# Kernel optimization log

Hardware: AMD Instinct MI355X
Metric: run time of the kernel (lower is better)

Reference implementation:

```python
import jax, jax.numpy as jnp
from jax import lax
import numpy as np

B, L, D_MODEL = 4, 2048, 1024
D_STATE, D_CONV, EXPAND = 16, 4, 2
D_INNER = EXPAND * D_MODEL          # 2048
DT_RANK = D_MODEL // 16             # 64
LN_EPS = 1e-5


def setup_inputs() -> dict:
    key = jax.random.key(0)
    ks = jax.random.split(key, 8)
    s = 0.02
    # S4D-real init for A_log, as in Mamba
    A_init = jnp.tile(jnp.arange(1, D_STATE + 1, dtype=jnp.float32), (D_INNER, 1))
    return {
        "x": jax.random.normal(ks[0], (B, L, D_MODEL), jnp.float32),
        "ln_g": jnp.ones((D_MODEL,), jnp.float32),
        "ln_b": jnp.zeros((D_MODEL,), jnp.float32),
        "W_in": jax.random.normal(ks[1], (D_MODEL, 2 * D_INNER), jnp.float32) * s,
        "conv_w": jax.random.normal(ks[2], (D_INNER, D_CONV), jnp.float32) * s,
        "conv_b": jnp.zeros((D_INNER,), jnp.float32),
        "W_x": jax.random.normal(ks[3], (D_INNER, DT_RANK + 2 * D_STATE), jnp.float32) * s,
        "W_dt": jax.random.normal(ks[4], (DT_RANK, D_INNER), jnp.float32) * s,
        "b_dt": jnp.full((D_INNER,), -4.6, jnp.float32),  # softplus(b_dt) ~ 0.01
        "A_log": jnp.log(A_init),
        "Dskip": jnp.ones((D_INNER,), jnp.float32),
        "W_out": jax.random.normal(ks[5], (D_INNER, D_MODEL), jnp.float32) * s,
    }


def _layer_norm(x, g, b):
    mu = jnp.mean(x, -1, keepdims=True)
    var = jnp.mean((x - mu) ** 2, -1, keepdims=True)
    return (x - mu) * lax.rsqrt(var + LN_EPS) * g + b


def _mamba_block(x, ln_g, ln_b, W_in, conv_w, conv_b, W_x, W_dt, b_dt, A_log, Dskip, W_out):
    b, l, _ = x.shape
    xn = _layer_norm(x, ln_g, ln_b)

    # in_proj -> (u, z), each (B, L, d_inner)
    xz = xn @ W_in
    u, z = jnp.split(xz, 2, axis=-1)

    # causal depthwise conv over L + SiLU
    u_t = u.transpose(0, 2, 1)                      # (B, d_inner, L)
    k = conv_w[:, None, :]                          # (d_inner, 1, d_conv)
    uc = lax.conv_general_dilated(
        u_t, k, (1,), [(D_CONV - 1, 0)],
        dimension_numbers=("NCH", "OIH", "NCH"),
        feature_group_count=D_INNER,
    ) + conv_b[None, :, None]
    uc = jax.nn.silu(uc).transpose(0, 2, 1)         # (B, L, d_inner)

    # input-dependent dt, B, C
    dbc = uc @ W_x                                  # (B, L, dt_rank + 2*d_state)
    dt_r = dbc[..., :DT_RANK]
    Bs = dbc[..., DT_RANK:DT_RANK + D_STATE]        # (B, L, d_state)
    Cs = dbc[..., DT_RANK + D_STATE:]               # (B, L, d_state)
    dt = jax.nn.softplus(dt_r @ W_dt + b_dt)        # (B, L, d_inner)

    A = -jnp.exp(A_log)                             # (d_inner, d_state)

    def step(h, ins):
        dt_t, B_t, C_t, u_t = ins                   # (b,di),(b,ds),(b,ds),(b,di)
        dA = jnp.exp(dt_t[..., None] * A)           # (b, di, ds)
        h = h * dA + (dt_t * u_t)[..., None] * B_t[:, None, :]
        y = jnp.einsum("bds,bs->bd", h, C_t)
        return h, y

    h0 = jnp.zeros((b, D_INNER, D_STATE), x.dtype)
    xs = (dt.transpose(1, 0, 2), Bs.transpose(1, 0, 2),
          Cs.transpose(1, 0, 2), uc.transpose(1, 0, 2))
    _, ys = lax.scan(step, h0, xs)                  # (L, B, d_inner)
    y = ys.transpose(1, 0, 2) + uc * Dskip          # D skip connection
    y = y * jax.nn.silu(z)                          # gate
    return x + y @ W_out                            # residual (dropout=0)


def reference(x, ln_g, ln_b, W_in, conv_w, conv_b, W_x, W_dt, b_dt, A_log, Dskip, W_out):
    return _mamba_block(x, ln_g, ln_b, W_in, conv_w, conv_b, W_x, W_dt, b_dt, A_log, Dskip, W_out)
```

## Files before the change

kernel.cpp:

```cpp
#include <hip/hip_runtime.h>
#include <hip/hip_bf16.h>

#define BB 4
#define LL 2048
#define DM 1024
#define DI 2048
#define DST 16
#define DTR 64
#define ROWS (BB*LL)
#define NC 32
#define CHUNK (LL/NC)

using bf16x8 = __attribute__((ext_vector_type(8))) __bf16;
using f32x4  = __attribute__((ext_vector_type(4))) float;

#define AS1 __attribute__((address_space(1)))
#define AS3 __attribute__((address_space(3)))

__global__ __launch_bounds__(256) void transpose_bf16_kernel(const float* __restrict__ src,
                                                             __hip_bfloat16* __restrict__ dst,
                                                             int R, int C, int Cpad) {
    __shared__ float t[32][33];
    const int c0 = blockIdx.x * 32, r0 = blockIdx.y * 32;
    const int tx = threadIdx.x & 31, ty = threadIdx.x >> 5;
    #pragma unroll
    for (int k = 0; k < 4; k++) {
        const int r = r0 + ty + 8 * k, c = c0 + tx;
        t[ty + 8 * k][tx] = (r < R && c < C) ? src[(size_t)r * C + c] : 0.f;
    }
    __syncthreads();
    #pragma unroll
    for (int k = 0; k < 4; k++) {
        const int c = c0 + ty + 8 * k, r = r0 + tx;
        if (c < Cpad && r < R) dst[(size_t)c * R + r] = __float2bfloat16(t[tx][ty + 8 * k]);
    }
}

__global__ __launch_bounds__(256) void ln_bf16_kernel(const float* __restrict__ x,
                                                      const float* __restrict__ g,
                                                      const float* __restrict__ bta,
                                                      __hip_bfloat16* __restrict__ xn) {
    const int row = blockIdx.x;
    const int tid = threadIdx.x;
    const float4 v = ((const float4*)(x + (size_t)row * DM))[tid];
    float s  = v.x + v.y + v.z + v.w;
    float sq = v.x*v.x + v.y*v.y + v.z*v.z + v.w*v.w;
    #pragma unroll
    for (int m = 1; m < 64; m <<= 1) {
        s  += __shfl_xor(s, m);
        sq += __shfl_xor(sq, m);
    }
    __shared__ float ss[4], ssq[4];
    const int w = tid >> 6;
    if ((tid & 63) == 0) { ss[w] = s; ssq[w] = sq; }
    __syncthreads();
    s  = ss[0] + ss[1] + ss[2] + ss[3];
    sq = ssq[0] + ssq[1] + ssq[2] + ssq[3];
    const float mu  = s * (1.f / DM);
    const float var = sq * (1.f / DM) - mu * mu;
    const float rs  = rsqrtf(var + 1e-5f);
    const float4 gv = ((const float4*)g)[tid];
    const float4 bv = ((const float4*)bta)[tid];
    __hip_bfloat16* op = xn + (size_t)row * DM + tid * 4;
    op[0] = __float2bfloat16((v.x - mu) * rs * gv.x + bv.x);
    op[1] = __float2bfloat16((v.y - mu) * rs * gv.y + bv.y);
    op[2] = __float2bfloat16((v.z - mu) * rs * gv.z + bv.z);
    op[3] = __float2bfloat16((v.w - mu) * rs * gv.w + bv.w);
}

template<int MODE>
__global__ __launch_bounds__(256) void mfma_gemm(const __hip_bfloat16* __restrict__ A,
                                                 const __hip_bfloat16* __restrict__ Bt,
                                                 float* __restrict__ O,
                                                 __hip_bfloat16* __restrict__ Oz,
                                                 __hip_bfloat16* __restrict__ Ozb,
                                                 const float* __restrict__ Add,
                                                 int K) {
    __shared__ __hip_bfloat16 As[2 * 128 * 32];
    __shared__ __hip_bfloat16 Bs[2 * 128 * 32];
    const int tid  = threadIdx.x;
    const int lane = tid & 63;
    const int w    = tid >> 6;

    const int nbx = gridDim.x, nby = gridDim.y;
    const int lid  = blockIdx.y * nbx + blockIdx.x;
    const int span = 8 * nbx;
    const int grp  = lid / span;
    const int fm0  = grp * 8;
    const int gsz  = min(nby - fm0, 8);
    const int by   = fm0 + (lid % gsz);
    const int bx   = (lid % span) / gsz;

    const int row0 = by * 128, col0 = bx * 128;
    const int wr0 = (w >> 1) * 64, wc0 = (w & 1) * 64;

    f32x4 acc[4][4];
    #pragma unroll
    for (int i = 0; i < 4; i++)
        #pragma unroll
        for (int j = 0; j < 4; j++) acc[i][j] = f32x4{0.f, 0.f, 0.f, 0.f};

    const int fm = lane & 15;
    const int fq = (lane >> 4) * 8;

    for (int k0 = 0; k0 < K; k0 += 64) {
        #pragma unroll
        for (int j = 0; j < 4; j++) {
            const int c   = w * 256 + j * 64 + lane;
            const int p   = c >> 9;
            const int row = (c >> 2) & 127;
            const int kq  = (c & 3) * 8;
            const int gk  = k0 + p * 32 + kq;
            __builtin_amdgcn_global_load_lds(
                (const AS1 unsigned int*)(A + (size_t)(row0 + row) * K + gk),
                (AS3 unsigned int*)(As + c * 8), 16, 0, 0);
            __builtin_amdgcn_global_load_lds(
                (const AS1 unsigned int*)(Bt + (size_t)(col0 + row) * K + gk),
                (AS3 unsigned int*)(Bs + c * 8), 16, 0, 0);
        }
        __syncthreads();
        #pragma unroll
        for (int half = 0; half < 2; half++) {
            bf16x8 af[4], bfr[4];
            #pragma unroll
            for (int i = 0; i < 4; i++)
                af[i] = *(const bf16x8*)&As[half * 4096 + (wr0 + i * 16 + fm) * 32 + fq];
            #pragma unroll
            for (int j = 0; j < 4; j++)
                bfr[j] = *(const bf16x8*)&Bs[half * 4096 + (wc0 + j * 16 + fm) * 32 + fq];
            #pragma unroll
            for (int i = 0; i < 4; i++)
                #pragma unroll
                for (int j = 0; j < 4; j++)
                    acc[i][j] = __builtin_amdgcn_mfma_f32_16x16x32_bf16(af[i], bfr[j], acc[i][j], 0, 0, 0);
        }
        __syncthreads();
    }

    #pragma unroll
    for (int i = 0; i < 4; i++) {
        #pragma unroll
        for (int j = 0; j < 4; j++) {
            #pragma unroll
            for (int r = 0; r < 4; r++) {
                const int row = row0 + wr0 + i * 16 + (lane >> 4) * 4 + r;
                const int col = col0 + wc0 + j * 16 + fm;
                const float v = acc[i][j][r];
                if (MODE == 0) {
                    if (col0 < DI) Oz[(size_t)row * DI + col] = __float2bfloat16(v);
                    else           Ozb[(size_t)row * DI + (col - DI)] = __float2bfloat16(v);
                } else if (MODE == 1) {
                    if (col >= DTR && col < DTR + 2 * DST)
                        O[(size_t)row * 128 + col] = v;
                    else if (col < DTR)
                        Oz[(size_t)row * DTR + col] = __float2bfloat16(v);
                } else if (MODE == 2) {
                    O[(size_t)row * DM + col] = v + Add[(size_t)row * DM + col];
                } else {
                    const float t  = v + Add[col];
                    const float sp = (t > 20.f) ? t : __logf(1.f + __expf(t));
                    Oz[(size_t)row * DI + col] = __float2bfloat16(sp);
                }
            }
        }
    }
}

__global__ __launch_bounds__(256) void conv_silu_kernel(const __hip_bfloat16* __restrict__ u,
                                                        const float* __restrict__ cw,
                                                        const float* __restrict__ cb,
                                                        __hip_bfloat16* __restrict__ uc) {
    const int d  = blockIdx.x * 256 + threadIdx.x;
    const int b  = blockIdx.z;
    const int l0 = blockIdx.y * 16;
    const float w0 = cw[d * 4 + 0], w1 = cw[d * 4 + 1];
    const float w2 = cw[d * 4 + 2], w3 = cw[d * 4 + 3];
    const float bias = cb[d];
    const __hip_bfloat16* up = u + (size_t)(b * LL) * DI + d;
    float x0 = (l0 - 3 >= 0) ? __bfloat162float(up[(size_t)(l0 - 3) * DI]) : 0.f;
    float x1 = (l0 - 2 >= 0) ? __bfloat162float(up[(size_t)(l0 - 2) * DI]) : 0.f;
    float x2 = (l0 - 1 >= 0) ? __bfloat162float(up[(size_t)(l0 - 1) * DI]) : 0.f;
    __hip_bfloat16* op = uc + (size_t)(b * LL + l0) * DI + d;
    #pragma unroll
    for (int i = 0; i < 16; i++) {
        const float x3 = __bfloat162float(up[(size_t)(l0 + i) * DI]);
        const float v  = bias + w0 * x0 + w1 * x1 + w2 * x2 + w3 * x3;
        const float sig = __builtin_amdgcn_rcpf(1.f + __expf(-v));
        op[(size_t)i * DI] = __float2bfloat16(v * sig);
        x0 = x1; x1 = x2; x2 = x3;
    }
}

__global__ __launch_bounds__(256) void scan_pass1_kernel(const __hip_bfloat16* __restrict__ dtb,
                                                         const __hip_bfloat16* __restrict__ uc,
                                                         const float* __restrict__ dbc,
                                                         const float* __restrict__ A_log,
                                                         float* __restrict__ hbuf,
                                                         float* __restrict__ Pbuf) {
    __shared__ float Bsh[CHUNK][16];
    const int tid = threadIdx.x;
    const int d   = blockIdx.x * 256 + tid;
    const int c   = blockIdx.y;
    const int b   = blockIdx.z;
    const size_t row0 = (size_t)b * LL + (size_t)c * CHUNK;

    {
        const int r = tid >> 2, j4 = (tid & 3) * 4;
        *(float4*)&Bsh[r][j4] = *(const float4*)(dbc + (row0 + r) * 128 + DTR + j4);
    }
    float a[DST];
    #pragma unroll
    for (int q = 0; q < 4; q++) {
        const float4 t = *(const float4*)(A_log + (size_t)d * DST + q * 4);
        a[q * 4 + 0] = -__expf(t.x); a[q * 4 + 1] = -__expf(t.y);
        a[q * 4 + 2] = -__expf(t.z); a[q * 4 + 3] = -__expf(t.w);
    }
    __syncthreads();

    const __hip_bfloat16* dtp = dtb + row0 * DI + d;
    const __hip_bfloat16* ucp = uc + row0 * DI + d;

    float h[DST];
    #pragma unroll
    for (int s = 0; s < DST; s++) h[s] = 0.f;
    float sdt = 0.f;
    float dtv = __bfloat162float(dtp[0]), ucv = __bfloat162float(ucp[0]);
    for (int l = 0; l < CHUNK; l++) {
        const int ln = (l + 1 < CHUNK) ? (l + 1) : l;
        const float dtn = __bfloat162float(dtp[(size_t)ln * DI]);
        const float ucn = __bfloat162float(ucp[(size_t)ln * DI]);
        const float dtu = dtv * ucv;
        sdt += dtv;
        #pragma unroll
        for (int s = 0; s < DST; s++) {
            const float dA = __expf(dtv * a[s]);
            h[s] = fmaf(h[s], dA, dtu * Bsh[l][s]);
        }
        dtv = dtn; ucv = ucn;
    }
    float* hp = hbuf + (((size_t)b * NC + c) * DI + d) * DST;
    float* pp = Pbuf + (((size_t)b * NC + c) * DI + d) * DST;
    #pragma unroll
    for (int q = 0; q < 4; q++) {
        *(float4*)&hp[q * 4] = float4{h[q*4+0], h[q*4+1], h[q*4+2], h[q*4+3]};
        *(float4*)&pp[q * 4] = float4{__expf(sdt * a[q*4+0]), __expf(sdt * a[q*4+1]),
                                      __expf(sdt * a[q*4+2]), __expf(sdt * a[q*4+3])};
    }
}

__global__ __launch_bounds__(256) void scan_combine_kernel(float* __restrict__ hbuf,
                                                           const float* __restrict__ Pbuf) {
    const size_t gid  = (size_t)blockIdx.x * 256 + threadIdx.x;
    const size_t b    = gid >> 15;
    const size_t d16s = gid & 32767;
    float H = 0.f;
    #pragma unroll
    for (int c = 0; c < NC; c++) {
        const size_t idx = (b * NC + c) * (DI * DST) + d16s;
        const float hc = hbuf[idx];
        const float Pc = Pbuf[idx];
        hbuf[idx] = H;
        H = hc + Pc * H;
    }
}

__global__ __launch_bounds__(256) void scan_pass3_kernel(const __hip_bfloat16* __restrict__ dtb,
                                                         __hip_bfloat16* uc,
                                                         const __hip_bfloat16* __restrict__ z,
                                                         const float* __restrict__ dbc,
                                                         const float* __restrict__ A_log,
                                                         const float* __restrict__ Dskip,
                                                         const float* __restrict__ hbuf) {
    __shared__ float BC[CHUNK][32];
    const int tid = threadIdx.x;
    const int d   = blockIdx.x * 256 + tid;
    const int c   = blockIdx.y;
    const int b   = blockIdx.z;
    const size_t row0 = (size_t)b * LL + (size_t)c * CHUNK;

    #pragma unroll
    for (int i = 0; i < 2; i++) {
        const int idx = i * 256 + tid;
        const int r = idx >> 3, j4 = (idx & 7) * 4;
        *(float4*)&BC[r][j4] = *(const float4*)(dbc + (row0 + r) * 128 + DTR + j4);
    }
    float a[DST];
    #pragma unroll
    for (int q = 0; q < 4; q++) {
        const float4 t = *(const float4*)(A_log + (size_t)d * DST + q * 4);
        a[q * 4 + 0] = -__expf(t.x); a[q * 4 + 1] = -__expf(t.y);
        a[q * 4 + 2] = -__expf(t.z); a[q * 4 + 3] = -__expf(t.w);
    }
    const float dsk = Dskip[d];
    __syncthreads();

    const __hip_bfloat16* dtp = dtb + row0 * DI + d;
    __hip_bfloat16* ucp = uc + row0 * DI + d;
    const __hip_bfloat16* zp = z + row0 * DI + d;

    float h[DST];
    {
        const float* hp = hbuf + (((size_t)b * NC + c) * DI + d) * DST;
        #pragma unroll
        for (int q = 0; q < 4; q++) {
            const float4 t = *(const float4*)&hp[q * 4];
            h[q*4+0] = t.x; h[q*4+1] = t.y; h[q*4+2] = t.z; h[q*4+3] = t.w;
        }
    }
    float dtv = __bfloat162float(dtp[0]);
    float ucv = __bfloat162float(ucp[0]);
    float zv  = __bfloat162float(zp[0]);
    for (int l = 0; l < CHUNK; l++) {
        const int ln = (l + 1 < CHUNK) ? (l + 1) : l;
        const float dtn = __bfloat162float(dtp[(size_t)ln * DI]);
        const float ucn = __bfloat162float(ucp[(size_t)ln * DI]);
        const float zn  = __bfloat162float(zp[(size_t)ln * DI]);
        const float dtu = dtv * ucv;
        float y = 0.f;
        #pragma unroll
        for (int s = 0; s < DST; s++) {
            const float dA = __expf(dtv * a[s]);
            h[s] = fmaf(h[s], dA, dtu * BC[l][s]);
            y = fmaf(h[s], BC[l][16 + s], y);
        }
        const float yt  = fmaf(ucv, dsk, y);
        const float sig = __builtin_amdgcn_rcpf(1.f + __expf(-zv));
        ucp[(size_t)l * DI] = __float2bfloat16(yt * (zv * sig));
        dtv = dtn; ucv = ucn; zv = zn;
    }
}

extern "C" void kernel_launch(void* const* d_in, const int* in_sizes, int n_in,
                              void* d_out, int out_size, void* d_ws, size_t ws_size,
                              hipStream_t stream) {
    const float* x      = (const float*)d_in[0];
    const float* ln_g   = (const float*)d_in[1];
    const float* ln_b   = (const float*)d_in[2];
    const float* W_in   = (const float*)d_in[3];
    const float* conv_w = (const float*)d_in[4];
    const float* conv_b = (const float*)d_in[5];
    const float* W_x    = (const float*)d_in[6];
    const float* W_dt   = (const float*)d_in[7];
    const float* b_dt   = (const float*)d_in[8];
    const float* A_log  = (const float*)d_in[9];
    const float* Dskip  = (const float*)d_in[10];
    const float* W_out  = (const float*)d_in[11];
    float* out = (float*)d_out;

    const size_t MB = 1024ull * 1024ull;
    char* wsb = (char*)d_ws;
    __hip_bfloat16* ub    = (__hip_bfloat16*)(wsb);
    __hip_bfloat16* z     = (__hip_bfloat16*)(wsb + 32 * MB);
    __hip_bfloat16* uc    = (__hip_bfloat16*)(wsb + 64 * MB);
    __hip_bfloat16* xn    = (__hip_bfloat16*)(wsb + 96 * MB);
    __hip_bfloat16* WinT  = (__hip_bfloat16*)(wsb + 112 * MB);
    __hip_bfloat16* WoutT = (__hip_bfloat16*)(wsb + 120 * MB);
    __hip_bfloat16* WxT   = (__hip_bfloat16*)(wsb + 124 * MB);
    float*          dbc   = (float*)(wsb + 125 * MB);
    float*          hbuf  = (float*)(wsb + 129 * MB);
    float*          Pbuf  = (float*)(wsb + 145 * MB);
    __hip_bfloat16* dbc64 = (__hip_bfloat16*)(wsb + 161 * MB);
    __hip_bfloat16* WdtT  = (__hip_bfloat16*)(wsb + 162 * MB);
    __hip_bfloat16* dtb   = ub;

    transpose_bf16_kernel<<<dim3(128, 32), 256, 0, stream>>>(W_in, WinT, DM, 2 * DI, 2 * DI);
    transpose_bf16_kernel<<<dim3(32, 64), 256, 0, stream>>>(W_out, WoutT, DI, DM, DM);
    transpose_bf16_kernel<<<dim3(4, 64), 256, 0, stream>>>(W_x, WxT, DI, 96, 128);
    transpose_bf16_kernel<<<dim3(64, 2), 256, 0, stream>>>(W_dt, WdtT, DTR, DI, DI);
    ln_bf16_kernel<<<ROWS, 256, 0, stream>>>(x, ln_g, ln_b, xn);
    mfma_gemm<0><<<dim3(32, 64), 256, 0, stream>>>(xn, WinT, nullptr, ub, z, nullptr, DM);
    conv_silu_kernel<<<dim3(DI / 256, LL / 16, BB), 256, 0, stream>>>(ub, conv_w, conv_b, uc);
    mfma_gemm<1><<<dim3(1, 64), 256, 0, stream>>>(uc, WxT, dbc, dbc64, nullptr, nullptr, DI);
    mfma_gemm<3><<<dim3(DI / 128, ROWS / 128), 256, 0, stream>>>(dbc64, WdtT, nullptr, dtb, nullptr, b_dt, DTR);
    scan_pass1_kernel<<<dim3(DI / 256, NC, BB), 256, 0, stream>>>(dtb, uc, dbc, A_log, hbuf, Pbuf);
    scan_combine_kernel<<<(BB * DI * DST) / 256, 256, 0, stream>>>(hbuf, Pbuf);
    scan_pass3_kernel<<<dim3(DI / 256, NC, BB), 256, 0, stream>>>(dtb, uc, z, dbc, A_log, Dskip, hbuf);
    mfma_gemm<2><<<dim3(DM / 128, ROWS / 128), 256, 0, stream>>>(uc, WoutT, out, nullptr, nullptr, x, DI);
}
```

Baseline: 459.9 us.

## Split-K the x_proj GEMM, swizzle LDS tiles, remap blocks per XCD, merge transposes

The narrow x_proj GEMM (64 blocks over K=2048) is split four ways along K into a partial buffer, and a separate reduce kernel sums the partials and writes dbc and dbc64. This is meant to fill more CUs. The GEMM's LDS layout gets an XOR swizzle on the k-quad index to reduce bank conflicts. Block-to-tile mapping now groups rows per XCD instead of the previous grouped raster. The four weight transposes become one launch. In exchange there is extra partial-buffer traffic and one more kernel launch.

```diff
diff --git a/kernel.cpp b/kernel.cpp
--- a/kernel.cpp
+++ b/kernel.cpp
@@ -17,22 +17,30 @@
 #define AS1 __attribute__((address_space(1)))
 #define AS3 __attribute__((address_space(3)))
 
-__global__ __launch_bounds__(256) void transpose_bf16_kernel(const float* __restrict__ src,
-                                                             __hip_bfloat16* __restrict__ dst,
-                                                             int R, int C, int Cpad) {
-    __shared__ float t[32][33];
-    const int c0 = blockIdx.x * 32, r0 = blockIdx.y * 32;
+__global__ __launch_bounds__(256) void transpose_all_kernel(
+        const float* __restrict__ Wi, const float* __restrict__ Wo,
+        const float* __restrict__ Wx, const float* __restrict__ Wd,
+        __hip_bfloat16* __restrict__ WiT, __hip_bfloat16* __restrict__ WoT,
+        __hip_bfloat16* __restrict__ WxT, __hip_bfloat16* __restrict__ WdT) {
+    const int t = blockIdx.x;
+    const float* src; __hip_bfloat16* dst; int R, C, Cpad, nx, idx;
+    if (t < 4096)      { src = Wi; dst = WiT; R = 1024; C = 4096; Cpad = 4096; nx = 128; idx = t; }
+    else if (t < 6144) { src = Wo; dst = WoT; R = 2048; C = 1024; Cpad = 1024; nx = 32;  idx = t - 4096; }
+    else if (t < 6400) { src = Wx; dst = WxT; R = 2048; C = 96;   Cpad = 128;  nx = 4;   idx = t - 6144; }
+    else               { src = Wd; dst = WdT; R = 64;   C = 2048; Cpad = 2048; nx = 64;  idx = t - 6400; }
+    __shared__ float tl[32][33];
+    const int c0 = (idx % nx) * 32, r0 = (idx / nx) * 32;
     const int tx = threadIdx.x & 31, ty = threadIdx.x >> 5;
     #pragma unroll
     for (int k = 0; k < 4; k++) {
         const int r = r0 + ty + 8 * k, c = c0 + tx;
-        t[ty + 8 * k][tx] = (r < R && c < C) ? src[(size_t)r * C + c] : 0.f;
+        tl[ty + 8 * k][tx] = (r < R && c < C) ? src[(size_t)r * C + c] : 0.f;
     }
     __syncthreads();
     #pragma unroll
     for (int k = 0; k < 4; k++) {
         const int c = c0 + ty + 8 * k, r = r0 + tx;
-        if (c < Cpad && r < R) dst[(size_t)c * R + r] = __float2bfloat16(t[tx][ty + 8 * k]);
+        if (c < Cpad && r < R) dst[(size_t)c * R + r] = __float2bfloat16(tl[tx][ty + 8 * k]);
     }
 }
 
@@ -75,7 +83,7 @@
                                                  __hip_bfloat16* __restrict__ Oz,
                                                  __hip_bfloat16* __restrict__ Ozb,
                                                  const float* __restrict__ Add,
-                                                 int K) {
+                                                 int Kstride, int klen) {
     __shared__ __hip_bfloat16 As[2 * 128 * 32];
     __shared__ __hip_bfloat16 Bs[2 * 128 * 32];
     const int tid  = threadIdx.x;
@@ -83,13 +91,11 @@
     const int w    = tid >> 6;
 
     const int nbx = gridDim.x, nby = gridDim.y;
-    const int lid  = blockIdx.y * nbx + blockIdx.x;
-    const int span = 8 * nbx;
-    const int grp  = lid / span;
-    const int fm0  = grp * 8;
-    const int gsz  = min(nby - fm0, 8);
-    const int by   = fm0 + (lid % gsz);
-    const int bx   = (lid % span) / gsz;
+    const int lid = blockIdx.y * nbx + blockIdx.x;
+    const int rpx = nby >> 3;
+    const int xcd = lid & 7, sl = lid >> 3;
+    const int by  = xcd * rpx + (sl % rpx);
+    const int bx  = sl / rpx;
 
     const int row0 = by * 128, col0 = bx * 128;
     const int wr0 = (w >> 1) * 64, wc0 = (w & 1) * 64;
@@ -100,22 +106,24 @@
         #pragma unroll
         for (int j = 0; j < 4; j++) acc[i][j] = f32x4{0.f, 0.f, 0.f, 0.f};
 
-    const int fm = lane & 15;
-    const int fq = (lane >> 4) * 8;
-
-    for (int k0 = 0; k0 < K; k0 += 64) {
+    const int fm  = lane & 15;
+    const int fqi = lane >> 4;
+    const int fqX = ((fqi ^ (fm & 3)) << 3);
+
+    const int kbeg = blockIdx.z * klen;
+    for (int k0 = kbeg; k0 < kbeg + klen; k0 += 64) {
         #pragma unroll
         for (int j = 0; j < 4; j++) {
             const int c   = w * 256 + j * 64 + lane;
             const int p   = c >> 9;
             const int row = (c >> 2) & 127;
-            const int kq  = (c & 3) * 8;
-            const int gk  = k0 + p * 32 + kq;
+            const int q   = (c & 3) ^ (row & 3);
+            const int gk  = k0 + p * 32 + q * 8;
             __builtin_amdgcn_global_load_lds(
-                (const AS1 unsigned int*)(A + (size_t)(row0 + row) * K + gk),
+                (const AS1 unsigned int*)(A + (size_t)(row0 + row) * Kstride + gk),
                 (AS3 unsigned int*)(As + c * 8), 16, 0, 0);
             __builtin_amdgcn_global_load_lds(
-                (const AS1 unsigned int*)(Bt + (size_t)(col0 + row) * K + gk),
+                (const AS1 unsigned int*)(Bt + (size_t)(col0 + row) * Kstride + gk),
                 (AS3 unsigned int*)(Bs + c * 8), 16, 0, 0);
         }
         __syncthreads();
@@ -124,10 +132,10 @@
             bf16x8 af[4], bfr[4];
             #pragma unroll
             for (int i = 0; i < 4; i++)
-                af[i] = *(const bf16x8*)&As[half * 4096 + (wr0 + i * 16 + fm) * 32 + fq];
+                af[i] = *(const bf16x8*)&As[half * 4096 + (wr0 + i * 16 + fm) * 32 + fqX];
             #pragma unroll
             for (int j = 0; j < 4; j++)
-                bfr[j] = *(const bf16x8*)&Bs[half * 4096 + (wc0 + j * 16 + fm) * 32 + fq];
+                bfr[j] = *(const bf16x8*)&Bs[half * 4096 + (wc0 + j * 16 + fm) * 32 + fqX];
             #pragma unroll
             for (int i = 0; i < 4; i++)
                 #pragma unroll
@@ -149,21 +157,32 @@
                 if (MODE == 0) {
                     if (col0 < DI) Oz[(size_t)row * DI + col] = __float2bfloat16(v);
                     else           Ozb[(size_t)row * DI + (col - DI)] = __float2bfloat16(v);
-                } else if (MODE == 1) {
-                    if (col >= DTR && col < DTR + 2 * DST)
-                        O[(size_t)row * 128 + col] = v;
-                    else if (col < DTR)
-                        Oz[(size_t)row * DTR + col] = __float2bfloat16(v);
                 } else if (MODE == 2) {
                     O[(size_t)row * DM + col] = v + Add[(size_t)row * DM + col];
-                } else {
+                } else if (MODE == 3) {
                     const float t  = v + Add[col];
                     const float sp = (t > 20.f) ? t : __logf(1.f + __expf(t));
                     Oz[(size_t)row * DI + col] = __float2bfloat16(sp);
+                } else {
+                    O[((size_t)blockIdx.z * ROWS + row) * 128 + col] = v;
                 }
             }
         }
     }
+}
+
+__global__ __launch_bounds__(256) void dbc_reduce_kernel(const float* __restrict__ pbuf,
+                                                         float* __restrict__ dbc,
+                                                         __hip_bfloat16* __restrict__ dbc64) {
+    const size_t gid = (size_t)blockIdx.x * 256 + threadIdx.x;
+    const int    col = gid & 127;
+    const size_t row = gid >> 7;
+    float sum = 0.f;
+    #pragma unroll
+    for (int sp = 0; sp < 4; sp++)
+        sum += pbuf[((size_t)sp * ROWS + row) * 128 + col];
+    if (col < DTR)                   dbc64[row * DTR + col] = __float2bfloat16(sum);
+    else if (col < DTR + 2 * DST)    dbc[row * 128 + col] = sum;
 }
 
 __global__ __launch_bounds__(256) void conv_silu_kernel(const __hip_bfloat16* __restrict__ u,
@@ -361,19 +380,23 @@
     float*          Pbuf  = (float*)(wsb + 145 * MB);
     __hip_bfloat16* dbc64 = (__hip_bfloat16*)(wsb + 161 * MB);
     __hip_bfloat16* WdtT  = (__hip_bfloat16*)(wsb + 162 * MB);
+    float*          pbuf  = (float*)(wsb + 163 * MB);
     __hip_bfloat16* dtb   = ub;
 
-    transpose_bf16_kernel<<<dim3(128, 32), 256, 0, stream>>>(W_in, WinT, DM, 2 * DI, 2 * DI);
-    transpose_bf16_kernel<<<dim3(32, 64), 256, 0, stream>>>(W_out, WoutT, DI, DM, DM);
-    transpose_bf16_kernel<<<dim3(4, 64), 256, 0, stream>>>(W_x, WxT, DI, 96, 128);
-    transpose_bf16_kernel<<<dim3(64, 2), 256, 0, stream>>>(W_dt, WdtT, DTR, DI, DI);
+    transpose_all_kernel<<<6528, 256, 0, stream>>>(W_in, W_out, W_x, W_dt,
+                                                   WinT, WoutT, WxT, WdtT);
     ln_bf16_kernel<<<ROWS, 256, 0, stream>>>(x, ln_g, ln_b, xn);
-    mfma_gemm<0><<<dim3(32, 64), 256, 0, stream>>>(xn, WinT, nullptr, ub, z, nullptr, DM);
+    mfma_gemm<0><<<dim3(32, 64), 256, 0, stream>>>(
+        xn, WinT, nullptr, ub, z, nullptr, DM, DM);
     conv_silu_kernel<<<dim3(DI / 256, LL / 16, BB), 256, 0, stream>>>(ub, conv_w, conv_b, uc);
-    mfma_gemm<1><<<dim3(1, 64), 256, 0, stream>>>(uc, WxT, dbc, dbc64, nullptr, nullptr, DI);
-    mfma_gemm<3><<<dim3(DI / 128, ROWS / 128), 256, 0, stream>>>(dbc64, WdtT, nullptr, dtb, nullptr, b_dt, DTR);
+    mfma_gemm<4><<<dim3(1, 64, 4), 256, 0, stream>>>(
+        uc, WxT, pbuf, nullptr, nullptr, nullptr, DI, DI / 4);
+    dbc_reduce_kernel<<<(ROWS * 128) / 256, 256, 0, stream>>>(pbuf, dbc, dbc64);
+    mfma_gemm<3><<<dim3(DI / 128, ROWS / 128), 256, 0, stream>>>(
+        dbc64, WdtT, nullptr, dtb, nullptr, b_dt, DTR, DTR);
     scan_pass1_kernel<<<dim3(DI / 256, NC, BB), 256, 0, stream>>>(dtb, uc, dbc, A_log, hbuf, Pbuf);
     scan_combine_kernel<<<(BB * DI * DST) / 256, 256, 0, stream>>>(hbuf, Pbuf);
     scan_pass3_kernel<<<dim3(DI / 256, NC, BB), 256, 0, stream>>>(dtb, uc, z, dbc, A_log, Dskip, hbuf);
-    mfma_gemm<2><<<dim3(DM / 128, ROWS / 128), 256, 0, stream>>>(uc, WoutT, out, nullptr, nullptr, x, DI);
-}
+    mfma_gemm<2><<<dim3(DM / 128, ROWS / 128), 256, 0, stream>>>(
+        uc, WoutT, out, nullptr, nullptr, x, DI, DI);
+}
```

Result: faster. 432.7 us (-5.9%).
